# Performance work log

Hardware: AMD Instinct MI355X
Metric: run time of the kernel (lower is better)

## Reference

```python
import jax, jax.numpy as jnp
import numpy as np

IGNORE_LABEL = 7
BETA = 1.0 / 9.0  # smooth-L1 beta from fastrcnn_loss


def setup_inputs() -> dict:
    key = jax.random.key(0)
    k = jax.random.split(key, 12)
    N, C, K, HM, G = 1024, 8, 17, 56, 256
    class_logits = jax.random.normal(k[0], (N, C), dtype=jnp.float32)
    box_regression = jax.random.normal(k[1], (N, C * 4), dtype=jnp.float32)
    regression_targets = jax.random.normal(k[2], (N, 4), dtype=jnp.float32) * 0.2
    # valid xyxy proposals in a ~1000px tile, widths/heights in [8, 64]
    x1 = jax.random.uniform(k[3], (N,)) * 900.0
    y1 = jax.random.uniform(k[4], (N,)) * 900.0
    w = 8.0 + jax.random.uniform(k[5], (N,)) * 56.0
    h = 8.0 + jax.random.uniform(k[6], (N,)) * 56.0
    proposals = jnp.stack([x1, y1, x1 + w, y1 + h], axis=1)
    # ground-truth keypoints: (x, y, visibility)
    kp_xy = jax.random.uniform(k[7], (G, K, 2)) * 1000.0
    kp_vis = (jax.random.uniform(k[8], (G, K, 1)) > 0.3).astype(jnp.float32)
    gt_keypoints = jnp.concatenate([kp_xy, kp_vis], axis=-1)
    keypoint_logits = jax.random.normal(k[9], (N, K, HM, HM), dtype=jnp.float32)
    labels = jax.random.randint(k[10], (N,), 0, C)
    keypoint_matched_idxs = jax.random.randint(k[11], (N,), 0, G)
    return {
        "class_logits": class_logits,
        "box_regression": box_regression,
        "regression_targets": regression_targets,
        "proposals": proposals,
        "gt_keypoints": gt_keypoints,
        "keypoint_logits": keypoint_logits,
        "labels": labels,
        "keypoint_matched_idxs": keypoint_matched_idxs,
    }


def _masked_ce(logits, targets, mask):
    # cross entropy averaged over masked entries (== F.cross_entropy on the subset)
    logp = jax.nn.log_softmax(logits, axis=-1)
    nll = -jnp.take_along_axis(logp, targets[:, None], axis=1)[:, 0]
    cnt = jnp.maximum(jnp.sum(mask.astype(logits.dtype)), 1.0)
    return jnp.sum(jnp.where(mask, nll, 0.0)) / cnt


def reference(class_logits, box_regression, regression_targets, proposals,
              gt_keypoints, keypoint_logits, labels, keypoint_matched_idxs):
    N, C = class_logits.shape
    # ---- fastrcnn_loss ----
    clkeep = labels != IGNORE_LABEL
    classification_loss = _masked_ce(class_logits, labels, clkeep)

    pos = labels > 0  # sampled_pos_inds_subset
    br = box_regression.reshape(N, C, 4)
    sel = jnp.take_along_axis(br, labels[:, None, None], axis=1)[:, 0, :]  # [N,4]
    d = sel - regression_targets
    ad = jnp.abs(d)
    sl1 = jnp.where(ad < BETA, 0.5 * d * d / BETA, ad - 0.5 * BETA)  # smooth_l1, sum
    box_loss = jnp.sum(jnp.where(pos[:, None], sl1, 0.0)) / N

    # ---- keypointrcnn_loss (keypoints_to_heatmap + CE over H*W bins) ----
    Nk, K, H, W = keypoint_logits.shape  # H == W == discretization_size
    kp = gt_keypoints[keypoint_matched_idxs]  # [N,K,3]
    ox, oy = proposals[:, 0:1], proposals[:, 1:2]
    sx = H / (proposals[:, 2:3] - proposals[:, 0:1])
    sy = H / (proposals[:, 3:4] - proposals[:, 1:2])
    kx, ky, vis = kp[..., 0], kp[..., 1], kp[..., 2]
    x = jnp.floor((kx - ox) * sx).astype(jnp.int32)
    y = jnp.floor((ky - oy) * sy).astype(jnp.int32)
    x = jnp.where(kx == proposals[:, 2:3], H - 1, x)
    y = jnp.where(ky == proposals[:, 3:4], H - 1, y)
    valid = (x >= 0) & (y >= 0) & (x < H) & (y < H) & (vis > 0)
    lin = (y * H + x) * valid.astype(jnp.int32)  # invalid entries -> bin 0 (masked out)
    kp_logits = keypoint_logits.reshape(Nk * K, H * W)
    keypoint_loss = _masked_ce(kp_logits, lin.reshape(-1), valid.reshape(-1))

    return jnp.stack([classification_loss, box_loss, keypoint_loss])
```

## Files before the change

### kernel.cpp

```cpp
#include <hip/hip_runtime.h>
#include <math.h>

#define K_KP 17
#define HM 56
#define HW (HM * HM)
#define N_ROWS 1024
#define NK_ROWS (N_ROWS * K_KP)
#define KP_META_BLOCKS (NK_ROWS / 256)
#define GRID (KP_META_BLOCKS + 1)
#define C_CLS 8
#define IGNORE_LABEL 7
#define BETA_C (1.0f / 9.0f)


__global__ __launch_bounds__(256) void roiheads_main(
    const float* __restrict__ class_logits,
    const float* __restrict__ box_regression,
    const float* __restrict__ regression_targets,
    const float* __restrict__ proposals,
    const float* __restrict__ gt_keypoints,
    const float* __restrict__ keypoint_logits,
    const int*   __restrict__ labels,
    const int*   __restrict__ kmi,
    float* __restrict__ ws)
{
    const int bid  = blockIdx.x;
    const int tid  = threadIdx.x;
    const int lane = tid & 63;
    const int wid  = tid >> 6;

    __shared__ int   q_r[256];
    __shared__ int   q_lin[256];
    __shared__ int   q_cnt;
    __shared__ float w0[4], w1[4], w2[4];

    float p0 = 0.0f, p1 = 0.0f, p2 = 0.0f, p3 = 0.0f, p4 = 0.0f;

    if (bid < KP_META_BLOCKS) {
        if (tid == 0) q_cnt = 0;
        __syncthreads();

        const int r = bid * 256 + tid;
        const int n = r / K_KP;
        const int k = r - n * K_KP;
        const int g = kmi[n];
        const float* kp = gt_keypoints + ((size_t)g * K_KP + k) * 3;
        const float kx  = kp[0];
        const float ky  = kp[1];
        const float vis = kp[2];
        const float4 pr = ((const float4*)proposals)[n];
        const float sx = (float)HM / (pr.z - pr.x);
        const float sy = (float)HM / (pr.w - pr.y);
        int xi = (int)floorf((kx - pr.x) * sx);
        int yi = (int)floorf((ky - pr.y) * sy);
        if (kx == pr.z) xi = HM - 1;
        if (ky == pr.w) yi = HM - 1;
        const bool valid = (xi >= 0) & (yi >= 0) & (xi < HM) & (yi < HM) & (vis > 0.0f);
        if (valid) {
            const int p = atomicAdd(&q_cnt, 1);
            q_r[p]   = r;
            q_lin[p] = yi * HM + xi;
        }
        __syncthreads();
        const int cnt = q_cnt;

        float my_s = 0.0f, my_c = 0.0f;
        for (int i = wid; i < cnt; i += 4) {
            const int rr = q_r[i];
            const float* row = keypoint_logits + (size_t)rr * HW;
            const float4* rp = (const float4*)row;
            float m = -INFINITY, s = 0.0f;
            #pragma unroll
            for (int it = 0; it < 13; ++it) {
                const int idx = it * 64 + lane;
                if (idx < HW / 4) {
                    const float4 v = rp[idx];
                    float vals[4] = {v.x, v.y, v.z, v.w};
                    #pragma unroll
                    for (int j = 0; j < 4; ++j) {
                        const float x = vals[j];
                        if (x > m) { s = s * expf(m - x) + 1.0f; m = x; }
                        else       { s += expf(x - m); }
                    }
                }
            }
            #pragma unroll
            for (int off = 32; off > 0; off >>= 1) {
                const float om = __shfl_down(m, off, 64);
                const float os = __shfl_down(s, off, 64);
                const float nm = fmaxf(m, om);
                s = s * expf(m - nm) + os * expf(om - nm);
                m = nm;
            }
            if (lane == 0) {
                const float xt = row[q_lin[i]];
                my_s += m + logf(s) - xt;
                my_c += 1.0f;
            }
        }
        if (lane == 0) { w0[wid] = my_s; w1[wid] = my_c; }
        __syncthreads();
        if (tid == 0) {
            p0 = w0[0] + w0[1] + w0[2] + w0[3];
            p1 = w1[0] + w1[1] + w1[2] + w1[3];
        }
    } else {
        float cls_part = 0.0f, keep_part = 0.0f, box_part = 0.0f;
        #pragma unroll
        for (int j = 0; j < 4; ++j) {
            const int n = j * 256 + tid;
            const int label = labels[n];
            const float* cl = class_logits + (size_t)n * C_CLS;
            float m = cl[0];
            #pragma unroll
            for (int c = 1; c < C_CLS; ++c) m = fmaxf(m, cl[c]);
            float s = 0.0f;
            #pragma unroll
            for (int c = 0; c < C_CLS; ++c) s += expf(cl[c] - m);
            const float nll  = m + logf(s) - cl[label];
            const float keep = (label != IGNORE_LABEL) ? 1.0f : 0.0f;
            cls_part  += keep * nll;
            keep_part += keep;
            if (label > 0) {
                #pragma unroll
                for (int c = 0; c < 4; ++c) {
                    const float d = box_regression[(size_t)n * 32 + label * 4 + c]
                                  - regression_targets[(size_t)n * 4 + c];
                    const float ad = fabsf(d);
                    box_part += (ad < BETA_C) ? 0.5f * d * d / BETA_C : ad - 0.5f * BETA_C;
                }
            }
        }
        #pragma unroll
        for (int off = 32; off > 0; off >>= 1) {
            cls_part  += __shfl_down(cls_part,  off, 64);
            keep_part += __shfl_down(keep_part, off, 64);
            box_part  += __shfl_down(box_part,  off, 64);
        }
        if (lane == 0) { w0[wid] = cls_part; w1[wid] = keep_part; w2[wid] = box_part; }
        __syncthreads();
        if (tid == 0) {
            p2 = w0[0] + w0[1] + w0[2] + w0[3];
            p3 = w1[0] + w1[1] + w1[2] + w1[3];
            p4 = w2[0] + w2[1] + w2[2] + w2[3];
        }
    }

    if (tid == 0) {
        float* slot = ws + (size_t)bid * 5;
        slot[0] = p0; slot[1] = p1; slot[2] = p2; slot[3] = p3; slot[4] = p4;
    }
}

__global__ __launch_bounds__(128) void roiheads_finalize(
    const float* __restrict__ ws, float* __restrict__ out)
{
    __shared__ float acc[5];
    const int tid = threadIdx.x;
    if (tid < 5) acc[tid] = 0.0f;
    __syncthreads();
    float v[5] = {0.0f, 0.0f, 0.0f, 0.0f, 0.0f};
    if (tid < GRID) {
        const float* slot = ws + (size_t)tid * 5;
        #pragma unroll
        for (int j = 0; j < 5; ++j) v[j] = slot[j];
    }
    #pragma unroll
    for (int j = 0; j < 5; ++j) atomicAdd(&acc[j], v[j]);
    __syncthreads();
    if (tid == 0) {
        out[0] = acc[2] / fmaxf(acc[3], 1.0f);
        out[1] = acc[4] / (float)N_ROWS;
        out[2] = acc[0] / fmaxf(acc[1], 1.0f);
    }
}

extern "C" void kernel_launch(void* const* d_in, const int* in_sizes, int n_in,
                              void* d_out, int out_size, void* d_ws, size_t ws_size,
                              hipStream_t stream) {
    const float* class_logits       = (const float*)d_in[0];
    const float* box_regression     = (const float*)d_in[1];
    const float* regression_targets = (const float*)d_in[2];
    const float* proposals          = (const float*)d_in[3];
    const float* gt_keypoints       = (const float*)d_in[4];
    const float* keypoint_logits    = (const float*)d_in[5];
    const int*   labels             = (const int*)d_in[6];
    const int*   kmi                = (const int*)d_in[7];
    float* ws  = (float*)d_ws;
    float* out = (float*)d_out;

    roiheads_main<<<GRID, 256, 0, stream>>>(
        class_logits, box_regression, regression_targets, proposals,
        gt_keypoints, keypoint_logits, labels, kmi, ws);

    roiheads_finalize<<<1, 128, 0, stream>>>(ws, out);
}
```

Before: 275.5 us.

## Buffer heatmap rows in registers for two-pass softmax; fuse finalize via flags

Each keypoint row is loaded once into 52 registers per lane. The log-sum-exp is then computed as a max pass followed by a sum pass, replacing the branchy online update that chained a dependent exp on every element. The goal is to issue all loads up front and break the serial dependency chain. The separate finalize launch is also removed: the class/box block spin-waits on per-block release flags and writes the outputs itself. The flags are never reset, so on later calls the reader can see stale partial sums from the previous run, and the spin-wait relies on every block being co-resident.

```diff
diff --git a/kernel.cpp b/kernel.cpp
--- a/kernel.cpp
+++ b/kernel.cpp
@@ -11,9 +11,10 @@
 #define C_CLS 8
 #define IGNORE_LABEL 7
 #define BETA_C (1.0f / 9.0f)
-
-
-__global__ __launch_bounds__(256) void roiheads_main(
+#define FLAG_MAGIC 0x13579BDFu
+
+
+__global__ __launch_bounds__(256) void roiheads_fused(
     const float* __restrict__ class_logits,
     const float* __restrict__ box_regression,
     const float* __restrict__ regression_targets,
@@ -22,21 +23,22 @@
     const float* __restrict__ keypoint_logits,
     const int*   __restrict__ labels,
     const int*   __restrict__ kmi,
-    float* __restrict__ ws)
+    float* __restrict__ ws,
+    float* __restrict__ out)
 {
     const int bid  = blockIdx.x;
     const int tid  = threadIdx.x;
     const int lane = tid & 63;
     const int wid  = tid >> 6;
 
-    __shared__ int   q_r[256];
-    __shared__ int   q_lin[256];
-    __shared__ int   q_cnt;
-    __shared__ float w0[4], w1[4], w2[4];
-
-    float p0 = 0.0f, p1 = 0.0f, p2 = 0.0f, p3 = 0.0f, p4 = 0.0f;
+    float* slots = ws;
+    unsigned int* flags = (unsigned int*)(ws + 2 * KP_META_BLOCKS);
 
     if (bid < KP_META_BLOCKS) {
+        __shared__ int   q_r[256];
+        __shared__ int   q_lin[256];
+        __shared__ int   q_cnt;
+        __shared__ float w0[4], w1[4];
         if (tid == 0) q_cnt = 0;
         __syncthreads();
 
@@ -69,29 +71,40 @@
             const int rr = q_r[i];
             const float* row = keypoint_logits + (size_t)rr * HW;
             const float4* rp = (const float4*)row;
-            float m = -INFINITY, s = 0.0f;
+
+            float xv[52];
             #pragma unroll
             for (int it = 0; it < 13; ++it) {
                 const int idx = it * 64 + lane;
-                if (idx < HW / 4) {
-                    const float4 v = rp[idx];
-                    float vals[4] = {v.x, v.y, v.z, v.w};
-                    #pragma unroll
-                    for (int j = 0; j < 4; ++j) {
-                        const float x = vals[j];
-                        if (x > m) { s = s * expf(m - x) + 1.0f; m = x; }
-                        else       { s += expf(x - m); }
-                    }
+                float4 v;
+                if (it < 12 || lane < (HW / 4 - 768)) {
+                    v = rp[idx];
+                } else {
+                    v = make_float4(-INFINITY, -INFINITY, -INFINITY, -INFINITY);
                 }
-            }
-            #pragma unroll
-            for (int off = 32; off > 0; off >>= 1) {
-                const float om = __shfl_down(m, off, 64);
-                const float os = __shfl_down(s, off, 64);
-                const float nm = fmaxf(m, om);
-                s = s * expf(m - nm) + os * expf(om - nm);
-                m = nm;
-            }
+                xv[it * 4 + 0] = v.x; xv[it * 4 + 1] = v.y;
+                xv[it * 4 + 2] = v.z; xv[it * 4 + 3] = v.w;
+            }
+            float m0 = -INFINITY, m1 = -INFINITY, m2 = -INFINITY, m3 = -INFINITY;
+            #pragma unroll
+            for (int j = 0; j < 13; ++j) {
+                m0 = fmaxf(m0, xv[4 * j + 0]); m1 = fmaxf(m1, xv[4 * j + 1]);
+                m2 = fmaxf(m2, xv[4 * j + 2]); m3 = fmaxf(m3, xv[4 * j + 3]);
+            }
+            float m = fmaxf(fmaxf(m0, m1), fmaxf(m2, m3));
+            #pragma unroll
+            for (int off = 32; off > 0; off >>= 1)
+                m = fmaxf(m, __shfl_xor(m, off, 64));
+            float s0 = 0.0f, s1 = 0.0f, s2 = 0.0f, s3 = 0.0f;
+            #pragma unroll
+            for (int j = 0; j < 13; ++j) {
+                s0 += expf(xv[4 * j + 0] - m); s1 += expf(xv[4 * j + 1] - m);
+                s2 += expf(xv[4 * j + 2] - m); s3 += expf(xv[4 * j + 3] - m);
+            }
+            float s = (s0 + s1) + (s2 + s3);
+            #pragma unroll
+            for (int off = 32; off > 0; off >>= 1)
+                s += __shfl_xor(s, off, 64);
             if (lane == 0) {
                 const float xt = row[q_lin[i]];
                 my_s += m + logf(s) - xt;
@@ -101,10 +114,16 @@
         if (lane == 0) { w0[wid] = my_s; w1[wid] = my_c; }
         __syncthreads();
         if (tid == 0) {
-            p0 = w0[0] + w0[1] + w0[2] + w0[3];
-            p1 = w1[0] + w1[1] + w1[2] + w1[3];
+            slots[bid * 2 + 0] = w0[0] + w0[1] + w0[2] + w0[3];
+            slots[bid * 2 + 1] = w1[0] + w1[1] + w1[2] + w1[3];
+            __hip_atomic_store(&flags[bid], FLAG_MAGIC,
+                               __ATOMIC_RELEASE, __HIP_MEMORY_SCOPE_AGENT);
         }
     } else {
+        __shared__ float red[5];
+        if (tid < 5) red[tid] = 0.0f;
+        __syncthreads();
+
         float cls_part = 0.0f, keep_part = 0.0f, box_part = 0.0f;
         #pragma unroll
         for (int j = 0; j < 4; ++j) {
@@ -137,41 +156,28 @@
             keep_part += __shfl_down(keep_part, off, 64);
             box_part  += __shfl_down(box_part,  off, 64);
         }
-        if (lane == 0) { w0[wid] = cls_part; w1[wid] = keep_part; w2[wid] = box_part; }
+        if (lane == 0) {
+            atomicAdd(&red[0], cls_part);
+            atomicAdd(&red[1], keep_part);
+            atomicAdd(&red[2], box_part);
+        }
+
+        if (tid < KP_META_BLOCKS) {
+            while (__hip_atomic_load(&flags[tid], __ATOMIC_ACQUIRE,
+                                     __HIP_MEMORY_SCOPE_AGENT) != FLAG_MAGIC) {
+                __builtin_amdgcn_s_sleep(1);
+            }
+            const float s0 = slots[tid * 2 + 0];
+            const float s1 = slots[tid * 2 + 1];
+            atomicAdd(&red[3], s0);
+            atomicAdd(&red[4], s1);
+        }
         __syncthreads();
         if (tid == 0) {
-            p2 = w0[0] + w0[1] + w0[2] + w0[3];
-            p3 = w1[0] + w1[1] + w1[2] + w1[3];
-            p4 = w2[0] + w2[1] + w2[2] + w2[3];
-        }
-    }
-
-    if (tid == 0) {
-        float* slot = ws + (size_t)bid * 5;
-        slot[0] = p0; slot[1] = p1; slot[2] = p2; slot[3] = p3; slot[4] = p4;
-    }
-}
-
-__global__ __launch_bounds__(128) void roiheads_finalize(
-    const float* __restrict__ ws, float* __restrict__ out)
-{
-    __shared__ float acc[5];
-    const int tid = threadIdx.x;
-    if (tid < 5) acc[tid] = 0.0f;
-    __syncthreads();
-    float v[5] = {0.0f, 0.0f, 0.0f, 0.0f, 0.0f};
-    if (tid < GRID) {
-        const float* slot = ws + (size_t)tid * 5;
-        #pragma unroll
-        for (int j = 0; j < 5; ++j) v[j] = slot[j];
-    }
-    #pragma unroll
-    for (int j = 0; j < 5; ++j) atomicAdd(&acc[j], v[j]);
-    __syncthreads();
-    if (tid == 0) {
-        out[0] = acc[2] / fmaxf(acc[3], 1.0f);
-        out[1] = acc[4] / (float)N_ROWS;
-        out[2] = acc[0] / fmaxf(acc[1], 1.0f);
+            out[0] = red[0] / fmaxf(red[1], 1.0f);
+            out[1] = red[2] / (float)N_ROWS;
+            out[2] = red[3] / fmaxf(red[4], 1.0f);
+        }
     }
 }
 
@@ -186,12 +192,9 @@
     const float* keypoint_logits    = (const float*)d_in[5];
     const int*   labels             = (const int*)d_in[6];
     const int*   kmi                = (const int*)d_in[7];
-    float* ws  = (float*)d_ws;
-    float* out = (float*)d_out;
-
-    roiheads_main<<<GRID, 256, 0, stream>>>(
+
+    roiheads_fused<<<GRID, 256, 0, stream>>>(
         class_logits, box_regression, regression_targets, proposals,
-        gt_keypoints, keypoint_logits, labels, kmi, ws);
-
-    roiheads_finalize<<<1, 128, 0, stream>>>(ws, out);
+        gt_keypoints, keypoint_logits, labels, kmi,
+        (float*)d_ws, (float*)d_out);
 }
```

After: 267.6 us. -2.9%, faster.
